# Kernel tuning notes

Measured on AMD Instinct MI355X. Metric: run time of the kernel, lower is better.

The kernel has to match this reference:

```python
import jax, jax.numpy as jnp
import numpy as np

B, S, E, D = 8, 4096, 16, 128   # batch, seq_len, n_experts, d_head
G = S // E                       # tokens routed to each expert


def setup_inputs() -> dict:
    key = jax.random.key(0)
    k1, k2, k3, k4 = jax.random.split(key, 4)
    Q = jax.random.normal(k1, (B, S, D), jnp.float32)
    K = jax.random.normal(k2, (B, S, D), jnp.float32)
    V = jax.random.normal(k3, (B, S, D), jnp.float32)
    # balanced hard routing: random permutation -> exactly G tokens per expert
    perm = jax.vmap(lambda k: jax.random.permutation(k, S))(jax.random.split(k4, B))  # [B,S]
    expert_ids = jnp.repeat(jnp.arange(E, dtype=jnp.int32), G)  # [S]
    assign = jnp.zeros((B, S), jnp.int32).at[jnp.arange(B)[:, None], perm].set(expert_ids[None, :])
    route_mat = jax.nn.one_hot(assign, E, dtype=jnp.float32)  # [B,S,E]
    # causal mask within each expert block; True = masked (filled with -inf)
    mask = jnp.triu(jnp.ones((G, G), dtype=bool), k=1)
    return {"Q": Q, "K": K, "V": V, "route_mat": route_mat, "mask": mask}


def reference(Q, K, V, route_mat, mask):
    # RowParallelMatmulWithMoE: gather each expert's routed tokens, block QK^T
    assign = jnp.argmax(route_mat, axis=-1)                 # [B,S]
    order = jnp.argsort(assign, axis=-1, stable=True)       # group tokens by expert
    idx = order.reshape(B, E, G)                            # [B,E,G]
    gather = jax.vmap(lambda x, i: x[i])                    # per-batch gather
    Qe, Ke, Ve = gather(Q, idx), gather(K, idx), gather(V, idx)  # [B,E,G,D]
    scores = jnp.einsum('begd,behd->begh', Qe, Ke)          # [B,E,G,G]
    dot = scores / jnp.sqrt(jnp.float32(D))
    m = mask[:G, :G]
    dot = jnp.where(m[None, None, :, :], -jnp.inf, dot)
    attn = jax.nn.softmax(dot, axis=-1)                     # dropout p=0.0 -> identity
    # ColumnParallelMatmulWithMoE, combine_head=False: per-expert AV
    X = jnp.einsum('begh,behd->begd', attn, Ve)             # [B,E,G,D]
    return X
```

## Files before the change

### kernel.cpp

```cpp
#include <hip/hip_runtime.h>
#include <hip/hip_bf16.h>

#define NB 8
#define NS 4096
#define NE 16
#define ND 128
#define NG 256

typedef float  f32x4 __attribute__((ext_vector_type(4)));
typedef short  s16x8 __attribute__((ext_vector_type(8)));
typedef short  s16x4 __attribute__((ext_vector_type(4)));

#define SCALE_LOG2E 0.12752749570528832f
#define NEGF (-1e30f)

__device__ __forceinline__ short f2bf(float f) {
  unsigned u = __builtin_bit_cast(unsigned, f);
  unsigned r = (u + 0x7fffu + ((u >> 16) & 1u)) >> 16;
  return (short)r;
}

template<int MAXT>
__device__ __forceinline__ void softmax_norm(f32x4 (&s)[MAXT]) {
  #pragma unroll
  for (int r = 0; r < 4; ++r) {
    float m = NEGF;
    #pragma unroll
    for (int ct = 0; ct < MAXT; ++ct) m = fmaxf(m, s[ct][r]);
    m = fmaxf(m, __shfl_xor(m, 1));
    m = fmaxf(m, __shfl_xor(m, 2));
    m = fmaxf(m, __shfl_xor(m, 4));
    m = fmaxf(m, __shfl_xor(m, 8));
    float sum = 0.f;
    #pragma unroll
    for (int ct = 0; ct < MAXT; ++ct) {
      float p = exp2f((s[ct][r] - m) * SCALE_LOG2E);
      s[ct][r] = p;
      sum += p;
    }
    sum += __shfl_xor(sum, 1);
    sum += __shfl_xor(sum, 2);
    sum += __shfl_xor(sum, 4);
    sum += __shfl_xor(sum, 8);
    float rinv = 1.0f / sum;
    #pragma unroll
    for (int ct = 0; ct < MAXT; ++ct) s[ct][r] *= rinv;
  }
}

template<int MAXT>
__device__ __forceinline__ void pv_store(const f32x4 (&s)[MAXT], int RT,
                                         const char* kvb, char* plw,
                                         float* outbase, int c15, int hi) {
  f32x4 o[8];
  #pragma unroll
  for (int dt = 0; dt < 8; ++dt) o[dt] = f32x4{0.f, 0.f, 0.f, 0.f};

  #pragma unroll
  for (int hc = 0; hc < MAXT / 4; ++hc) {
    if (hc * 4 <= RT) {
      #pragma unroll
      for (int cr = 0; cr < 4; ++cr) {
        const int ct = hc * 4 + cr;
        #pragma unroll
        for (int r = 0; r < 4; ++r) {
          float pv = (ct <= RT) ? s[ct][r] : 0.0f;
          int gl = hi * 4 + r;
          int byte = gl * 128 + (((cr * 16 + c15) * 2) ^ ((gl & 7) << 4));
          *(short*)(plw + byte) = f2bf(pv);
        }
      }
      #pragma unroll
      for (int kb = 0; kb < 2; ++kb) {
        int abyte = c15 * 128 + (((kb * 32 + hi * 8) * 2) ^ ((c15 & 7) << 4));
        s16x8 pf = *(const s16x8*)(plw + abyte);
        #pragma unroll
        for (int dt = 0; dt < 8; ++dt) {
          int d = dt * 16 + c15;
          int hof = hc * 64 + kb * 32 + hi * 8;
          int vbyte = d * 512 + ((hof * 2) ^ ((d & 7) << 4));
          s16x8 vf = *(const s16x8*)(kvb + vbyte);
          o[dt] = __builtin_amdgcn_mfma_f32_16x16x32_bf16(pf, vf, o[dt], 0, 0, 0);
        }
      }
    }
  }
  #pragma unroll
  for (int dt = 0; dt < 8; ++dt) {
    #pragma unroll
    for (int r = 0; r < 4; ++r)
      outbase[(size_t)(hi * 4 + r) * ND + dt * 16 + c15] = o[dt][r];
  }
}

__global__ __launch_bounds__(256, 1) void sattn_kernel(
    const float* __restrict__ Qg, const float* __restrict__ Kg,
    const float* __restrict__ Vg, const float* __restrict__ RM,
    float* __restrict__ Out) {
  __shared__ int idx[NG];
  __shared__ __align__(16) short kv[NG * ND];
  __shared__ __align__(16) short plds[4][16 * 64];

  const int tid = threadIdx.x;
  const int lane = tid & 63;
  const int w = tid >> 6;
  const int c15 = lane & 15;
  const int hi = lane >> 4;

  const int bid = blockIdx.x;
  const int be = bid >> 1;
  const int jhalf = bid & 1;
  const int b = be >> 4;
  const int e = be & 15;

  {
    int* cnt = (int*)kv;
    const float* rmb = RM + (size_t)b * NS * NE + e;
    unsigned mbits = 0;
    int cloc = 0;
    #pragma unroll
    for (int i = 0; i < 16; ++i) {
      bool m = rmb[(size_t)(tid * 16 + i) * NE] > 0.5f;
      mbits |= (m ? 1u : 0u) << i;
      cloc += m ? 1 : 0;
    }
    cnt[tid] = cloc;
    __syncthreads();
    for (int off = 1; off < 256; off <<= 1) {
      int v = cnt[tid];
      int add = (tid >= off) ? cnt[tid - off] : 0;
      __syncthreads();
      cnt[tid] = v + add;
      __syncthreads();
    }
    int pos = cnt[tid] - cloc;
    for (int i = 0; i < 16; ++i)
      if (mbits & (1u << i)) idx[pos++] = tid * 16 + i;
    __syncthreads();
  }

  {
    const int row_off = tid >> 5;
    const int c4 = tid & 31;
    const float* kbase = Kg + (size_t)b * NS * ND;
    #pragma unroll 4
    for (int r0 = 0; r0 < NG; r0 += 8) {
      int h = r0 + row_off;
      int tok = idx[h];
      float4 v = *(const float4*)(kbase + (size_t)tok * ND + c4 * 4);
      s16x4 p;
      p[0] = f2bf(v.x); p[1] = f2bf(v.y); p[2] = f2bf(v.z); p[3] = f2bf(v.w);
      int byte = h * 256 + ((c4 * 8) ^ ((h & 7) << 4));
      *(s16x4*)((char*)kv + byte) = p;
    }
  }

  const int pairIdx = jhalf * 4 + w;
  const int RTa = pairIdx;
  const int RTb = 15 - pairIdx;

  s16x8 qf[2][4];
  #pragma unroll
  for (int t = 0; t < 2; ++t) {
    const int RT = t ? RTb : RTa;
    const int g = RT * 16 + c15;
    const float* qrow = Qg + ((size_t)b * NS + idx[g]) * ND;
    #pragma unroll
    for (int kb = 0; kb < 4; ++kb) {
      const int d0 = kb * 32 + hi * 8;
      float4 x = *(const float4*)(qrow + d0);
      float4 y = *(const float4*)(qrow + d0 + 4);
      s16x8 q;
      q[0] = f2bf(x.x); q[1] = f2bf(x.y); q[2] = f2bf(x.z); q[3] = f2bf(x.w);
      q[4] = f2bf(y.x); q[5] = f2bf(y.y); q[6] = f2bf(y.z); q[7] = f2bf(y.w);
      qf[t][kb] = q;
    }
  }
  __syncthreads();

  f32x4 sA[8], sB[16];
  #pragma unroll
  for (int ct = 0; ct < 8; ++ct) {
    f32x4 acc = f32x4{0.f, 0.f, 0.f, 0.f};
    if (ct <= RTa) {
      #pragma unroll
      for (int kb = 0; kb < 4; ++kb) {
        int h = ct * 16 + c15;
        int byte = h * 256 + (((kb * 32 + hi * 8) * 2) ^ ((h & 7) << 4));
        s16x8 kf = *(const s16x8*)((const char*)kv + byte);
        acc = __builtin_amdgcn_mfma_f32_16x16x32_bf16(qf[0][kb], kf, acc, 0, 0, 0);
      }
      if (ct == RTa) {
        #pragma unroll
        for (int r = 0; r < 4; ++r)
          if (c15 > hi * 4 + r) acc[r] = NEGF;
      }
    } else {
      acc = f32x4{NEGF, NEGF, NEGF, NEGF};
    }
    sA[ct] = acc;
  }
  #pragma unroll
  for (int ct = 0; ct < 16; ++ct) {
    f32x4 acc = f32x4{0.f, 0.f, 0.f, 0.f};
    if (ct <= RTb) {
      #pragma unroll
      for (int kb = 0; kb < 4; ++kb) {
        int h = ct * 16 + c15;
        int byte = h * 256 + (((kb * 32 + hi * 8) * 2) ^ ((h & 7) << 4));
        s16x8 kf = *(const s16x8*)((const char*)kv + byte);
        acc = __builtin_amdgcn_mfma_f32_16x16x32_bf16(qf[1][kb], kf, acc, 0, 0, 0);
      }
      if (ct == RTb) {
        #pragma unroll
        for (int r = 0; r < 4; ++r)
          if (c15 > hi * 4 + r) acc[r] = NEGF;
      }
    } else {
      acc = f32x4{NEGF, NEGF, NEGF, NEGF};
    }
    sB[ct] = acc;
  }

  softmax_norm<8>(sA);
  softmax_norm<16>(sB);

  __syncthreads();

  {
    const int row = tid;
    const float* vrow = Vg + ((size_t)b * NS + idx[row]) * ND;
    #pragma unroll 4
    for (int p4 = 0; p4 < 32; ++p4) {
      float4 v = *(const float4*)(vrow + p4 * 4);
      #pragma unroll
      for (int i = 0; i < 4; ++i) {
        int d = p4 * 4 + i;
        float val = (i == 0) ? v.x : (i == 1) ? v.y : (i == 2) ? v.z : v.w;
        int byte = d * 512 + ((row * 2) ^ ((d & 7) << 4));
        *(short*)((char*)kv + byte) = f2bf(val);
      }
    }
  }
  __syncthreads();

  char* plw = (char*)plds[w];
  float* oa = Out + ((size_t)be * NG + RTa * 16) * ND;
  pv_store<8>(sA, RTa, (const char*)kv, plw, oa, c15, hi);
  float* ob = Out + ((size_t)be * NG + RTb * 16) * ND;
  pv_store<16>(sB, RTb, (const char*)kv, plw, ob, c15, hi);
}

extern "C" void kernel_launch(void* const* d_in, const int* in_sizes, int n_in,
                              void* d_out, int out_size, void* d_ws, size_t ws_size,
                              hipStream_t stream) {
  const float* Q  = (const float*)d_in[0];
  const float* K  = (const float*)d_in[1];
  const float* V  = (const float*)d_in[2];
  const float* RM = (const float*)d_in[3];
  float* Out = (float*)d_out;
  sattn_kernel<<<dim3(NB * NE * 2), dim3(256), 0, stream>>>(Q, K, V, RM, Out);
}
```

Measured before the change: 113.5 us.

## Split routing index build into separate kernel and quarter work per attention block

Moves the per-expert prefix-scan index construction into its own gather kernel that writes indices to workspace. The attention kernel now uses four blocks per (batch, expert) instead of two, each wave owning one balanced row tile, and loads only the K rows that tile range needs. Launch bounds allow two blocks per CU. This removes the routing scan that every attention block previously repeated and raises parallelism, at the cost of an extra launch and more redundant V staging across blocks.

```diff
diff --git a/kernel.cpp b/kernel.cpp
--- a/kernel.cpp
+++ b/kernel.cpp
@@ -20,20 +20,130 @@
   return (short)r;
 }
 
-template<int MAXT>
-__device__ __forceinline__ void softmax_norm(f32x4 (&s)[MAXT]) {
+__global__ __launch_bounds__(256) void gather_kernel(const float* __restrict__ RM,
+                                                     int* __restrict__ idx_out) {
+  __shared__ int cnt[256];
+  const int tid = threadIdx.x;
+  const int be = blockIdx.x;
+  const int b = be >> 4;
+  const int e = be & 15;
+  const float* rmb = RM + (size_t)b * NS * NE + e;
+  unsigned mbits = 0;
+  int cloc = 0;
+  #pragma unroll
+  for (int i = 0; i < 16; ++i) {
+    bool m = rmb[(size_t)(tid * 16 + i) * NE] > 0.5f;
+    mbits |= (m ? 1u : 0u) << i;
+    cloc += m ? 1 : 0;
+  }
+  cnt[tid] = cloc;
+  __syncthreads();
+  for (int off = 1; off < 256; off <<= 1) {
+    int v = cnt[tid];
+    int add = (tid >= off) ? cnt[tid - off] : 0;
+    __syncthreads();
+    cnt[tid] = v + add;
+    __syncthreads();
+  }
+  int pos = cnt[tid] - cloc;
+  int* ob = idx_out + (size_t)be * NG;
+  for (int i = 0; i < 16; ++i)
+    if (mbits & (1u << i)) ob[pos++] = tid * 16 + i;
+}
+
+__global__ __launch_bounds__(256, 2) void sattn_kernel(
+    const float* __restrict__ Qg, const float* __restrict__ Kg,
+    const float* __restrict__ Vg, const int* __restrict__ IdxW,
+    float* __restrict__ Out) {
+  __shared__ int idx[NG];
+  __shared__ __align__(16) short kv[NG * ND];
+  __shared__ __align__(16) short plds[4][16 * 64];
+
+  const int tid = threadIdx.x;
+  const int lane = tid & 63;
+  const int w = tid >> 6;
+  const int c15 = lane & 15;
+  const int hi = lane >> 4;
+
+  const int bid = blockIdx.x;
+  const int be = bid >> 2;
+  const int j = bid & 3;
+  const int b = be >> 4;
+
+  const int RT = (w == 0) ? j : (w == 1) ? (7 - j) : (w == 2) ? (8 + j) : (15 - j);
+  const int R = (16 - j) * 16;
+
+  idx[tid] = IdxW[(size_t)be * NG + tid];
+  __syncthreads();
+
+  s16x8 qf[4];
+  {
+    const int g = RT * 16 + c15;
+    const float* qrow = Qg + ((size_t)b * NS + idx[g]) * ND;
+    #pragma unroll
+    for (int kb = 0; kb < 4; ++kb) {
+      const int d0 = kb * 32 + hi * 8;
+      float4 x = *(const float4*)(qrow + d0);
+      float4 y = *(const float4*)(qrow + d0 + 4);
+      s16x8 q;
+      q[0] = f2bf(x.x); q[1] = f2bf(x.y); q[2] = f2bf(x.z); q[3] = f2bf(x.w);
+      q[4] = f2bf(y.x); q[5] = f2bf(y.y); q[6] = f2bf(y.z); q[7] = f2bf(y.w);
+      qf[kb] = q;
+    }
+  }
+
+  {
+    const int row_off = tid >> 5;
+    const int c4 = tid & 31;
+    const float* kbase = Kg + (size_t)b * NS * ND;
+    #pragma unroll 4
+    for (int r0 = 0; r0 < R; r0 += 8) {
+      int h = r0 + row_off;
+      int tok = idx[h];
+      float4 v = *(const float4*)(kbase + (size_t)tok * ND + c4 * 4);
+      s16x4 p;
+      p[0] = f2bf(v.x); p[1] = f2bf(v.y); p[2] = f2bf(v.z); p[3] = f2bf(v.w);
+      int byte = h * 256 + ((c4 * 8) ^ ((h & 7) << 4));
+      *(s16x4*)((char*)kv + byte) = p;
+    }
+  }
+  __syncthreads();
+
+  f32x4 s[16];
+  #pragma unroll
+  for (int ct = 0; ct < 16; ++ct) {
+    f32x4 acc = f32x4{0.f, 0.f, 0.f, 0.f};
+    if (ct <= RT) {
+      #pragma unroll
+      for (int kb = 0; kb < 4; ++kb) {
+        int h = ct * 16 + c15;
+        int byte = h * 256 + (((kb * 32 + hi * 8) * 2) ^ ((h & 7) << 4));
+        s16x8 kf = *(const s16x8*)((const char*)kv + byte);
+        acc = __builtin_amdgcn_mfma_f32_16x16x32_bf16(qf[kb], kf, acc, 0, 0, 0);
+      }
+      if (ct == RT) {
+        #pragma unroll
+        for (int r = 0; r < 4; ++r)
+          if (c15 > hi * 4 + r) acc[r] = NEGF;
+      }
+    } else {
+      acc = f32x4{NEGF, NEGF, NEGF, NEGF};
+    }
+    s[ct] = acc;
+  }
+
   #pragma unroll
   for (int r = 0; r < 4; ++r) {
     float m = NEGF;
     #pragma unroll
-    for (int ct = 0; ct < MAXT; ++ct) m = fmaxf(m, s[ct][r]);
+    for (int ct = 0; ct < 16; ++ct) m = fmaxf(m, s[ct][r]);
     m = fmaxf(m, __shfl_xor(m, 1));
     m = fmaxf(m, __shfl_xor(m, 2));
     m = fmaxf(m, __shfl_xor(m, 4));
     m = fmaxf(m, __shfl_xor(m, 8));
     float sum = 0.f;
     #pragma unroll
-    for (int ct = 0; ct < MAXT; ++ct) {
+    for (int ct = 0; ct < 16; ++ct) {
       float p = exp2f((s[ct][r] - m) * SCALE_LOG2E);
       s[ct][r] = p;
       sum += p;
@@ -44,30 +154,44 @@
     sum += __shfl_xor(sum, 8);
     float rinv = 1.0f / sum;
     #pragma unroll
-    for (int ct = 0; ct < MAXT; ++ct) s[ct][r] *= rinv;
-  }
-}
-
-template<int MAXT>
-__device__ __forceinline__ void pv_store(const f32x4 (&s)[MAXT], int RT,
-                                         const char* kvb, char* plw,
-                                         float* outbase, int c15, int hi) {
+    for (int ct = 0; ct < 16; ++ct) s[ct][r] *= rinv;
+  }
+
+  __syncthreads();
+
+  {
+    const int row = tid;
+    const float* vrow = Vg + ((size_t)b * NS + idx[row]) * ND;
+    #pragma unroll 4
+    for (int p4 = 0; p4 < 32; ++p4) {
+      float4 v = *(const float4*)(vrow + p4 * 4);
+      #pragma unroll
+      for (int i = 0; i < 4; ++i) {
+        int d = p4 * 4 + i;
+        float val = (i == 0) ? v.x : (i == 1) ? v.y : (i == 2) ? v.z : v.w;
+        int byte = d * 512 + ((row * 2) ^ ((d & 7) << 4));
+        *(short*)((char*)kv + byte) = f2bf(val);
+      }
+    }
+  }
+  __syncthreads();
+
+  char* plw = (char*)plds[w];
   f32x4 o[8];
   #pragma unroll
   for (int dt = 0; dt < 8; ++dt) o[dt] = f32x4{0.f, 0.f, 0.f, 0.f};
 
   #pragma unroll
-  for (int hc = 0; hc < MAXT / 4; ++hc) {
+  for (int hc = 0; hc < 4; ++hc) {
     if (hc * 4 <= RT) {
       #pragma unroll
       for (int cr = 0; cr < 4; ++cr) {
         const int ct = hc * 4 + cr;
         #pragma unroll
         for (int r = 0; r < 4; ++r) {
-          float pv = (ct <= RT) ? s[ct][r] : 0.0f;
           int gl = hi * 4 + r;
           int byte = gl * 128 + (((cr * 16 + c15) * 2) ^ ((gl & 7) << 4));
-          *(short*)(plw + byte) = f2bf(pv);
+          *(short*)(plw + byte) = f2bf(s[ct][r]);
         }
       }
       #pragma unroll
@@ -79,176 +203,20 @@
           int d = dt * 16 + c15;
           int hof = hc * 64 + kb * 32 + hi * 8;
           int vbyte = d * 512 + ((hof * 2) ^ ((d & 7) << 4));
-          s16x8 vf = *(const s16x8*)(kvb + vbyte);
+          s16x8 vf = *(const s16x8*)((const char*)kv + vbyte);
           o[dt] = __builtin_amdgcn_mfma_f32_16x16x32_bf16(pf, vf, o[dt], 0, 0, 0);
         }
       }
     }
   }
+
+  float* outbase = Out + ((size_t)be * NG + RT * 16) * ND;
   #pragma unroll
   for (int dt = 0; dt < 8; ++dt) {
     #pragma unroll
     for (int r = 0; r < 4; ++r)
       outbase[(size_t)(hi * 4 + r) * ND + dt * 16 + c15] = o[dt][r];
   }
-}
-
-__global__ __launch_bounds__(256, 1) void sattn_kernel(
-    const float* __restrict__ Qg, const float* __restrict__ Kg,
-    const float* __restrict__ Vg, const float* __restrict__ RM,
-    float* __restrict__ Out) {
-  __shared__ int idx[NG];
-  __shared__ __align__(16) short kv[NG * ND];
-  __shared__ __align__(16) short plds[4][16 * 64];
-
-  const int tid = threadIdx.x;
-  const int lane = tid & 63;
-  const int w = tid >> 6;
-  const int c15 = lane & 15;
-  const int hi = lane >> 4;
-
-  const int bid = blockIdx.x;
-  const int be = bid >> 1;
-  const int jhalf = bid & 1;
-  const int b = be >> 4;
-  const int e = be & 15;
-
-  {
-    int* cnt = (int*)kv;
-    const float* rmb = RM + (size_t)b * NS * NE + e;
-    unsigned mbits = 0;
-    int cloc = 0;
-    #pragma unroll
-    for (int i = 0; i < 16; ++i) {
-      bool m = rmb[(size_t)(tid * 16 + i) * NE] > 0.5f;
-      mbits |= (m ? 1u : 0u) << i;
-      cloc += m ? 1 : 0;
-    }
-    cnt[tid] = cloc;
-    __syncthreads();
-    for (int off = 1; off < 256; off <<= 1) {
-      int v = cnt[tid];
-      int add = (tid >= off) ? cnt[tid - off] : 0;
-      __syncthreads();
-      cnt[tid] = v + add;
-      __syncthreads();
-    }
-    int pos = cnt[tid] - cloc;
-    for (int i = 0; i < 16; ++i)
-      if (mbits & (1u << i)) idx[pos++] = tid * 16 + i;
-    __syncthreads();
-  }
-
-  {
-    const int row_off = tid >> 5;
-    const int c4 = tid & 31;
-    const float* kbase = Kg + (size_t)b * NS * ND;
-    #pragma unroll 4
-    for (int r0 = 0; r0 < NG; r0 += 8) {
-      int h = r0 + row_off;
-      int tok = idx[h];
-      float4 v = *(const float4*)(kbase + (size_t)tok * ND + c4 * 4);
-      s16x4 p;
-      p[0] = f2bf(v.x); p[1] = f2bf(v.y); p[2] = f2bf(v.z); p[3] = f2bf(v.w);
-      int byte = h * 256 + ((c4 * 8) ^ ((h & 7) << 4));
-      *(s16x4*)((char*)kv + byte) = p;
-    }
-  }
-
-  const int pairIdx = jhalf * 4 + w;
-  const int RTa = pairIdx;
-  const int RTb = 15 - pairIdx;
-
-  s16x8 qf[2][4];
-  #pragma unroll
-  for (int t = 0; t < 2; ++t) {
-    const int RT = t ? RTb : RTa;
-    const int g = RT * 16 + c15;
-    const float* qrow = Qg + ((size_t)b * NS + idx[g]) * ND;
-    #pragma unroll
-    for (int kb = 0; kb < 4; ++kb) {
-      const int d0 = kb * 32 + hi * 8;
-      float4 x = *(const float4*)(qrow + d0);
-      float4 y = *(const float4*)(qrow + d0 + 4);
-      s16x8 q;
-      q[0] = f2bf(x.x); q[1] = f2bf(x.y); q[2] = f2bf(x.z); q[3] = f2bf(x.w);
-      q[4] = f2bf(y.x); q[5] = f2bf(y.y); q[6] = f2bf(y.z); q[7] = f2bf(y.w);
-      qf[t][kb] = q;
-    }
-  }
-  __syncthreads();
-
-  f32x4 sA[8], sB[16];
-  #pragma unroll
-  for (int ct = 0; ct < 8; ++ct) {
-    f32x4 acc = f32x4{0.f, 0.f, 0.f, 0.f};
-    if (ct <= RTa) {
-      #pragma unroll
-      for (int kb = 0; kb < 4; ++kb) {
-        int h = ct * 16 + c15;
-        int byte = h * 256 + (((kb * 32 + hi * 8) * 2) ^ ((h & 7) << 4));
-        s16x8 kf = *(const s16x8*)((const char*)kv + byte);
-        acc = __builtin_amdgcn_mfma_f32_16x16x32_bf16(qf[0][kb], kf, acc, 0, 0, 0);
-      }
-      if (ct == RTa) {
-        #pragma unroll
-        for (int r = 0; r < 4; ++r)
-          if (c15 > hi * 4 + r) acc[r] = NEGF;
-      }
-    } else {
-      acc = f32x4{NEGF, NEGF, NEGF, NEGF};
-    }
-    sA[ct] = acc;
-  }
-  #pragma unroll
-  for (int ct = 0; ct < 16; ++ct) {
-    f32x4 acc = f32x4{0.f, 0.f, 0.f, 0.f};
-    if (ct <= RTb) {
-      #pragma unroll
-      for (int kb = 0; kb < 4; ++kb) {
-        int h = ct * 16 + c15;
-        int byte = h * 256 + (((kb * 32 + hi * 8) * 2) ^ ((h & 7) << 4));
-        s16x8 kf = *(const s16x8*)((const char*)kv + byte);
-        acc = __builtin_amdgcn_mfma_f32_16x16x32_bf16(qf[1][kb], kf, acc, 0, 0, 0);
-      }
-      if (ct == RTb) {
-        #pragma unroll
-        for (int r = 0; r < 4; ++r)
-          if (c15 > hi * 4 + r) acc[r] = NEGF;
-      }
-    } else {
-      acc = f32x4{NEGF, NEGF, NEGF, NEGF};
-    }
-    sB[ct] = acc;
-  }
-
-  softmax_norm<8>(sA);
-  softmax_norm<16>(sB);
-
-  __syncthreads();
-
-  {
-    const int row = tid;
-    const float* vrow = Vg + ((size_t)b * NS + idx[row]) * ND;
-    #pragma unroll 4
-    for (int p4 = 0; p4 < 32; ++p4) {
-      float4 v = *(const float4*)(vrow + p4 * 4);
-      #pragma unroll
-      for (int i = 0; i < 4; ++i) {
-        int d = p4 * 4 + i;
-        float val = (i == 0) ? v.x : (i == 1) ? v.y : (i == 2) ? v.z : v.w;
-        int byte = d * 512 + ((row * 2) ^ ((d & 7) << 4));
-        *(short*)((char*)kv + byte) = f2bf(val);
-      }
-    }
-  }
-  __syncthreads();
-
-  char* plw = (char*)plds[w];
-  float* oa = Out + ((size_t)be * NG + RTa * 16) * ND;
-  pv_store<8>(sA, RTa, (const char*)kv, plw, oa, c15, hi);
-  float* ob = Out + ((size_t)be * NG + RTb * 16) * ND;
-  pv_store<16>(sB, RTb, (const char*)kv, plw, ob, c15, hi);
 }
 
 extern "C" void kernel_launch(void* const* d_in, const int* in_sizes, int n_in,
@@ -259,5 +227,8 @@
   const float* V  = (const float*)d_in[2];
   const float* RM = (const float*)d_in[3];
   float* Out = (float*)d_out;
-  sattn_kernel<<<dim3(NB * NE * 2), dim3(256), 0, stream>>>(Q, K, V, RM, Out);
-}
+  int* idx_ws = (int*)d_ws;
+
+  gather_kernel<<<dim3(NB * NE), dim3(256), 0, stream>>>(RM, idx_ws);
+  sattn_kernel<<<dim3(NB * NE * 4), dim3(256), 0, stream>>>(Q, K, V, idx_ws, Out);
+}
```

New measurement: 121.1 us. 6.6% more time.
